# Kernel optimization log

Hardware: AMD Instinct MI355X
Metric: run time of the kernel (lower is better)

Reference implementation:

```python
import jax, jax.numpy as jnp
import numpy as np

B, T, N_EMBD, HEAD = 8, 2048, 1024, 64


def setup_inputs() -> dict:
    key = jax.random.key(0)
    kx, kq, kk, kv = jax.random.split(key, 4)
    s = 1.0 / np.sqrt(N_EMBD)
    return {
        "x": jax.random.normal(kx, (B, T, N_EMBD), dtype=jnp.float32),
        "Wq": jax.random.normal(kq, (N_EMBD, HEAD), dtype=jnp.float32) * s,
        "Wk": jax.random.normal(kk, (N_EMBD, HEAD), dtype=jnp.float32) * s,
        "Wv": jax.random.normal(kv, (N_EMBD, HEAD), dtype=jnp.float32) * s,
    }


def reference(x, Wq, Wk, Wv):
    # x: [B, T, C] with C = n_embd
    Bs, Ts, C = x.shape
    q = jnp.einsum('btc,ch->bth', x, Wq)  # [B,T,H]
    k = jnp.einsum('btc,ch->bth', x, Wk)
    v = jnp.einsum('btc,ch->bth', x, Wv)
    # NOTE: original scales by C**-0.5 where C = n_embd (input dim), not head_size
    scale = jnp.asarray(C, x.dtype) ** -0.5
    wei = jnp.einsum('bth,bsh->bts', q, k) * scale  # [B,T,T]
    causal = jnp.tril(jnp.ones((Ts, Ts), dtype=bool))
    wei = jnp.where(causal, wei, jnp.asarray(-jnp.inf, wei.dtype))
    wei = jax.nn.softmax(wei, axis=-1)
    out = jnp.einsum('bts,bsh->bth', wei, v)  # [B,T,H]
    return out
```

## Files before the change

kernel.cpp:

```cpp
#include <hip/hip_runtime.h>
#include <hip/hip_bf16.h>
#include <math.h>

#define B_ 8
#define T_ 2048
#define C_ 1024
#define H_ 64

typedef __attribute__((ext_vector_type(8))) __bf16 bf16x8;
typedef __attribute__((ext_vector_type(4))) float f32x4;

static __device__ inline unsigned short f2bf_u(float f) {
    __bf16 b = (__bf16)f;
    return __builtin_bit_cast(unsigned short, b);
}
static __device__ inline unsigned int pack2(float lo, float hi) {
    return (unsigned int)f2bf_u(lo) | ((unsigned int)f2bf_u(hi) << 16);
}
static __device__ inline bf16x8 cvt8(float4 a, float4 b) {
    bf16x8 w;
    w[0] = (__bf16)a.x; w[1] = (__bf16)a.y; w[2] = (__bf16)a.z; w[3] = (__bf16)a.w;
    w[4] = (__bf16)b.x; w[5] = (__bf16)b.y; w[6] = (__bf16)b.z; w[7] = (__bf16)b.w;
    return w;
}

__global__ void prep_w_kernel(const float* __restrict__ Wq,
                              const float* __restrict__ Wk,
                              const float* __restrict__ Wv,
                              unsigned short* __restrict__ Wp) {
    int idx = blockIdx.x * 256 + threadIdx.x;
    if (idx >= C_ * 192) return;
    int k = idx / 192;
    int n = idx % 192;
    const float* W = (n < 64) ? Wq : (n < 128) ? Wk : Wv;
    float val = W[k * 64 + (n & 63)];
    Wp[((size_t)(k >> 5) * 192 + n) * 32 + (k & 31)] = f2bf_u(val);
}

#define XSTR 264
__global__ __launch_bounds__(256, 4) void proj_kernel(
        const float* __restrict__ x, const unsigned short* __restrict__ Wp,
        unsigned short* __restrict__ q, unsigned short* __restrict__ k,
        unsigned short* __restrict__ vT) {
    __shared__ unsigned short xb[2][16][XSTR];
    const int wave = threadIdx.x >> 6;
    const int lane = threadIdx.x & 63;
    const int col  = lane & 15;
    const int quad = lane >> 4;
    const int row0 = blockIdx.x * 16;
    const int n0   = wave * 48;

    const int srow = threadIdx.x >> 4;
    const int sf   = (threadIdx.x & 15) * 16;
    const float* sb = x + (size_t)(row0 + srow) * C_ + sf;

    f32x4 acc[3];
    #pragma unroll
    for (int i = 0; i < 3; i++) acc[i] = (f32x4){0.f, 0.f, 0.f, 0.f};

    {
        float4 t0 = *(const float4*)(sb + 0),  t1 = *(const float4*)(sb + 4);
        float4 t2 = *(const float4*)(sb + 8),  t3 = *(const float4*)(sb + 12);
        *(bf16x8*)&xb[0][srow][sf]     = cvt8(t0, t1);
        *(bf16x8*)&xb[0][srow][sf + 8] = cvt8(t2, t3);
    }
    float4 l0 = *(const float4*)(sb + 256), l1 = *(const float4*)(sb + 260);
    float4 l2 = *(const float4*)(sb + 264), l3 = *(const float4*)(sb + 268);

    const unsigned short* wb = Wp + (size_t)(n0 + col) * 32 + quad * 8;
    bf16x8 bcur0 = *(const bf16x8*)(wb);
    bf16x8 bcur1 = *(const bf16x8*)(wb + 16 * 32);
    bf16x8 bcur2 = *(const bf16x8*)(wb + 32 * 32);
    __syncthreads();

    for (int p = 0; p < 4; ++p) {
        float4 f0, f1, f2, f3;
        if (p + 2 < 4) {
            const float* s2 = sb + (p + 2) * 256;
            f0 = *(const float4*)(s2 + 0);  f1 = *(const float4*)(s2 + 4);
            f2 = *(const float4*)(s2 + 8);  f3 = *(const float4*)(s2 + 12);
        }
        #pragma unroll
        for (int kt = 0; kt < 8; ++kt) {
            const int ktg = p * 8 + kt;
            bf16x8 bn0, bn1, bn2;
            if (ktg + 1 < 32) {
                const unsigned short* wn = wb + (size_t)(ktg + 1) * 192 * 32;
                bn0 = *(const bf16x8*)(wn);
                bn1 = *(const bf16x8*)(wn + 16 * 32);
                bn2 = *(const bf16x8*)(wn + 32 * 32);
            }
            bf16x8 a = *(const bf16x8*)&xb[p & 1][col][kt * 32 + quad * 8];
            acc[0] = __builtin_amdgcn_mfma_f32_16x16x32_bf16(a, bcur0, acc[0], 0, 0, 0);
            acc[1] = __builtin_amdgcn_mfma_f32_16x16x32_bf16(a, bcur1, acc[1], 0, 0, 0);
            acc[2] = __builtin_amdgcn_mfma_f32_16x16x32_bf16(a, bcur2, acc[2], 0, 0, 0);
            bcur0 = bn0; bcur1 = bn1; bcur2 = bn2;
        }
        if (p + 1 < 4) {
            unsigned short* d = &xb[(p + 1) & 1][srow][sf];
            *(bf16x8*)(d)     = cvt8(l0, l1);
            *(bf16x8*)(d + 8) = cvt8(l2, l3);
            l0 = f0; l1 = f1; l2 = f2; l3 = f3;
        }
        __syncthreads();
    }

    #pragma unroll
    for (int nt = 0; nt < 3; nt++) {
        f32x4 s = acc[nt];
        int c = n0 + nt * 16;
        int g = c >> 6;
        if (g < 2) {
            unsigned short* dst = (g == 0) ? q : k;
            int cc = (c & 63) + col;
            int grow = row0 + quad * 4;
            #pragma unroll
            for (int r = 0; r < 4; r++)
                dst[(size_t)(grow + r) * 64 + cc] = f2bf_u(s[r]);
        } else {
            int hh = (c - 128) + col;
            int bi = row0 >> 11, trow = (row0 & 2047) + quad * 4;
            ushort4 pk;
            pk.x = f2bf_u(s[0]); pk.y = f2bf_u(s[1]);
            pk.z = f2bf_u(s[2]); pk.w = f2bf_u(s[3]);
            *(ushort4*)(vT + ((size_t)bi * 64 + hh) * T_ + trow) = pk;
        }
    }
}

__global__ __launch_bounds__(512, 2) void attn_kernel(
        const unsigned short* __restrict__ q, const unsigned short* __restrict__ k,
        const unsigned short* __restrict__ vT, float* __restrict__ out) {
    __shared__ unsigned int tbuf[8][2][16 * 20];
    __shared__ float so[8][16][68];
    __shared__ float sl[8][16];
    const int wave = threadIdx.x >> 6;
    const int lane = threadIdx.x & 63;
    const int col  = lane & 15;
    const int quad = lane >> 4;
    const int bi = blockIdx.x & 7;
    const int ti = 127 - (blockIdx.x >> 3);
    const int t0 = ti * 16;
    const unsigned short* qb = q  + (size_t)bi * T_ * 64;
    const unsigned short* kb = k  + (size_t)bi * T_ * 64;
    const unsigned short* vb = vT + (size_t)bi * 64 * T_;

    bf16x8 qf0 = *(const bf16x8*)(qb + (size_t)(t0 + col) * 64 + quad * 8);
    bf16x8 qf1 = *(const bf16x8*)(qb + (size_t)(t0 + col) * 64 + 32 + quad * 8);

    f32x4 o[4];
    #pragma unroll
    for (int i = 0; i < 4; i++) o[i] = (f32x4){0.f, 0.f, 0.f, 0.f};
    float lacc = 0.f;
    const float cs = 0.03125f * 1.44269504088896f;
    const int qrow = t0 + col;

    const int nit = (t0 + 47) >> 5;
    const int ci  = (nit + 7) >> 3;
    const int it0 = wave * ci;
    const int it1 = min(it0 + ci, nit);

    for (int it = it0; it < it1; ++it) {
        const int s0 = it * 32;
        bf16x8 kf00 = *(const bf16x8*)(kb + (size_t)(s0 + col) * 64 + quad * 8);
        bf16x8 kf01 = *(const bf16x8*)(kb + (size_t)(s0 + col) * 64 + 32 + quad * 8);
        bf16x8 kf10 = *(const bf16x8*)(kb + (size_t)(s0 + 16 + col) * 64 + quad * 8);
        bf16x8 kf11 = *(const bf16x8*)(kb + (size_t)(s0 + 16 + col) * 64 + 32 + quad * 8);
        f32x4 sa = (f32x4){0.f, 0.f, 0.f, 0.f};
        f32x4 sb2 = (f32x4){0.f, 0.f, 0.f, 0.f};
        sa  = __builtin_amdgcn_mfma_f32_16x16x32_bf16(kf00, qf0, sa, 0, 0, 0);
        sa  = __builtin_amdgcn_mfma_f32_16x16x32_bf16(kf01, qf1, sa, 0, 0, 0);
        sb2 = __builtin_amdgcn_mfma_f32_16x16x32_bf16(kf10, qf0, sb2, 0, 0, 0);
        sb2 = __builtin_amdgcn_mfma_f32_16x16x32_bf16(kf11, qf1, sb2, 0, 0, 0);

        float pa[4], pb[4];
        #pragma unroll
        for (int r = 0; r < 4; r++) {
            int ka = s0 + quad * 4 + r;
            pa[r] = (ka      <= qrow) ? exp2f(sa[r]  * cs) : 0.f;
            pb[r] = (ka + 16 <= qrow) ? exp2f(sb2[r] * cs) : 0.f;
            lacc += pa[r] + pb[r];
        }
        unsigned int* tb = &tbuf[wave][it & 1][0];
        *(uint2*)&tb[col * 20 + 2 * quad] =
            make_uint2(pack2(pa[0], pa[1]), pack2(pa[2], pa[3]));
        *(uint2*)&tb[col * 20 + 8 + 2 * quad] =
            make_uint2(pack2(pb[0], pb[1]), pack2(pb[2], pb[3]));
        bf16x8 pf = *(const bf16x8*)&tb[col * 20 + 4 * quad];
        #pragma unroll
        for (int ht = 0; ht < 4; ht++) {
            bf16x8 vf = *(const bf16x8*)(vb + (size_t)(ht * 16 + col) * T_ + s0 + quad * 8);
            o[ht] = __builtin_amdgcn_mfma_f32_16x16x32_bf16(vf, pf, o[ht], 0, 0, 0);
        }
    }

    lacc += __shfl_xor(lacc, 16);
    lacc += __shfl_xor(lacc, 32);
    if (quad == 0) sl[wave][col] = lacc;
    #pragma unroll
    for (int ht = 0; ht < 4; ht++)
        *(f32x4*)&so[wave][col][ht * 16 + quad * 4] = o[ht];
    __syncthreads();

    for (int e = threadIdx.x; e < 1024; e += 512) {
        int qq = e >> 6, h = e & 63;
        float L = 0.f, val = 0.f;
        #pragma unroll
        for (int w = 0; w < 8; w++) { L += sl[w][qq]; val += so[w][qq][h]; }
        out[((size_t)bi * T_ + t0 + qq) * 64 + h] = val / L;
    }
}

extern "C" void kernel_launch(void* const* d_in, const int* in_sizes, int n_in,
                              void* d_out, int out_size, void* d_ws, size_t ws_size,
                              hipStream_t stream) {
    const float* x  = (const float*)d_in[0];
    const float* Wq = (const float*)d_in[1];
    const float* Wk = (const float*)d_in[2];
    const float* Wv = (const float*)d_in[3];
    float* out = (float*)d_out;

    unsigned short* Wp  = (unsigned short*)d_ws;
    unsigned short* qws = (unsigned short*)((char*)d_ws + 0x60000);
    unsigned short* kws = (unsigned short*)((char*)d_ws + 0x60000 + 0x200000);
    unsigned short* vws = (unsigned short*)((char*)d_ws + 0x60000 + 0x400000);

    prep_w_kernel<<<(C_ * 192 + 255) / 256, 256, 0, stream>>>(Wq, Wk, Wv, Wp);
    proj_kernel<<<(B_ * T_) / 16, 256, 0, stream>>>(x, Wp, qws, kws, vws);
    attn_kernel<<<(B_ * T_) / 16, 512, 0, stream>>>(qws, kws, vws, out);
}
```

Before: 159.2 us.

## Stage x via direct global-to-LDS loads and prefetch K/V in attention

The projection kernel now stages raw fp32 x tiles into a triple-buffered LDS ring with global_load_lds and converts to bf16 at fragment-read time. This removes the register round-trip and the separate convert-and-store step, but doubles the LDS footprint and lowers the occupancy bound to 3. The attention kernel software-pipelines K and V fragment loads one iteration ahead, skips Q loads for idle waves, and raises its occupancy hint to 4. The extra prefetch registers add register pressure.

```diff
diff --git a/kernel.cpp b/kernel.cpp
--- a/kernel.cpp
+++ b/kernel.cpp
@@ -37,12 +37,12 @@
     Wp[((size_t)(k >> 5) * 192 + n) * 32 + (k & 31)] = f2bf_u(val);
 }
 
-#define XSTR 264
-__global__ __launch_bounds__(256, 4) void proj_kernel(
+#define XROWB 1040
+__global__ __launch_bounds__(256, 3) void proj_kernel(
         const float* __restrict__ x, const unsigned short* __restrict__ Wp,
         unsigned short* __restrict__ q, unsigned short* __restrict__ k,
         unsigned short* __restrict__ vT) {
-    __shared__ unsigned short xb[2][16][XSTR];
+    __shared__ __align__(16) char xraw[3][16][XROWB];
     const int wave = threadIdx.x >> 6;
     const int lane = threadIdx.x & 63;
     const int col  = lane & 15;
@@ -50,23 +50,24 @@
     const int row0 = blockIdx.x * 16;
     const int n0   = wave * 48;
 
-    const int srow = threadIdx.x >> 4;
-    const int sf   = (threadIdx.x & 15) * 16;
-    const float* sb = x + (size_t)(row0 + srow) * C_ + sf;
+    auto stage = [&](int p, int buf) {
+        #pragma unroll
+        for (int i = 0; i < 4; i++) {
+            int r = wave * 4 + i;
+            const float* src = x + (size_t)(row0 + r) * C_ + p * 256 + lane * 4;
+            __builtin_amdgcn_global_load_lds(
+                (const __attribute__((address_space(1))) unsigned int*)src,
+                (__attribute__((address_space(3))) unsigned int*)&xraw[buf][r][0],
+                16, 0, 0);
+        }
+    };
 
     f32x4 acc[3];
     #pragma unroll
     for (int i = 0; i < 3; i++) acc[i] = (f32x4){0.f, 0.f, 0.f, 0.f};
 
-    {
-        float4 t0 = *(const float4*)(sb + 0),  t1 = *(const float4*)(sb + 4);
-        float4 t2 = *(const float4*)(sb + 8),  t3 = *(const float4*)(sb + 12);
-        *(bf16x8*)&xb[0][srow][sf]     = cvt8(t0, t1);
-        *(bf16x8*)&xb[0][srow][sf + 8] = cvt8(t2, t3);
-    }
-    float4 l0 = *(const float4*)(sb + 256), l1 = *(const float4*)(sb + 260);
-    float4 l2 = *(const float4*)(sb + 264), l3 = *(const float4*)(sb + 268);
-
+    stage(0, 0);
+    stage(1, 1);
     const unsigned short* wb = Wp + (size_t)(n0 + col) * 32 + quad * 8;
     bf16x8 bcur0 = *(const bf16x8*)(wb);
     bf16x8 bcur1 = *(const bf16x8*)(wb + 16 * 32);
@@ -74,12 +75,8 @@
     __syncthreads();
 
     for (int p = 0; p < 4; ++p) {
-        float4 f0, f1, f2, f3;
-        if (p + 2 < 4) {
-            const float* s2 = sb + (p + 2) * 256;
-            f0 = *(const float4*)(s2 + 0);  f1 = *(const float4*)(s2 + 4);
-            f2 = *(const float4*)(s2 + 8);  f3 = *(const float4*)(s2 + 12);
-        }
+        if (p + 2 < 4) stage(p + 2, (p + 2) % 3);
+        const char* abase = &xraw[p % 3][col][quad * 32];
         #pragma unroll
         for (int kt = 0; kt < 8; ++kt) {
             const int ktg = p * 8 + kt;
@@ -90,17 +87,13 @@
                 bn1 = *(const bf16x8*)(wn + 16 * 32);
                 bn2 = *(const bf16x8*)(wn + 32 * 32);
             }
-            bf16x8 a = *(const bf16x8*)&xb[p & 1][col][kt * 32 + quad * 8];
+            float4 u0 = *(const float4*)(abase + kt * 128);
+            float4 u1 = *(const float4*)(abase + kt * 128 + 16);
+            bf16x8 a = cvt8(u0, u1);
             acc[0] = __builtin_amdgcn_mfma_f32_16x16x32_bf16(a, bcur0, acc[0], 0, 0, 0);
             acc[1] = __builtin_amdgcn_mfma_f32_16x16x32_bf16(a, bcur1, acc[1], 0, 0, 0);
             acc[2] = __builtin_amdgcn_mfma_f32_16x16x32_bf16(a, bcur2, acc[2], 0, 0, 0);
             bcur0 = bn0; bcur1 = bn1; bcur2 = bn2;
-        }
-        if (p + 1 < 4) {
-            unsigned short* d = &xb[(p + 1) & 1][srow][sf];
-            *(bf16x8*)(d)     = cvt8(l0, l1);
-            *(bf16x8*)(d + 8) = cvt8(l2, l3);
-            l0 = f0; l1 = f1; l2 = f2; l3 = f3;
         }
         __syncthreads();
     }
@@ -128,7 +121,7 @@
     }
 }
 
-__global__ __launch_bounds__(512, 2) void attn_kernel(
+__global__ __launch_bounds__(512, 4) void attn_kernel(
         const unsigned short* __restrict__ q, const unsigned short* __restrict__ k,
         const unsigned short* __restrict__ vT, float* __restrict__ out) {
     __shared__ unsigned int tbuf[8][2][16 * 20];
@@ -145,9 +138,6 @@
     const unsigned short* kb = k  + (size_t)bi * T_ * 64;
     const unsigned short* vb = vT + (size_t)bi * 64 * T_;
 
-    bf16x8 qf0 = *(const bf16x8*)(qb + (size_t)(t0 + col) * 64 + quad * 8);
-    bf16x8 qf1 = *(const bf16x8*)(qb + (size_t)(t0 + col) * 64 + 32 + quad * 8);
-
     f32x4 o[4];
     #pragma unroll
     for (int i = 0; i < 4; i++) o[i] = (f32x4){0.f, 0.f, 0.f, 0.f};
@@ -160,37 +150,60 @@
     const int it0 = wave * ci;
     const int it1 = min(it0 + ci, nit);
 
-    for (int it = it0; it < it1; ++it) {
-        const int s0 = it * 32;
-        bf16x8 kf00 = *(const bf16x8*)(kb + (size_t)(s0 + col) * 64 + quad * 8);
-        bf16x8 kf01 = *(const bf16x8*)(kb + (size_t)(s0 + col) * 64 + 32 + quad * 8);
-        bf16x8 kf10 = *(const bf16x8*)(kb + (size_t)(s0 + 16 + col) * 64 + quad * 8);
-        bf16x8 kf11 = *(const bf16x8*)(kb + (size_t)(s0 + 16 + col) * 64 + 32 + quad * 8);
-        f32x4 sa = (f32x4){0.f, 0.f, 0.f, 0.f};
-        f32x4 sb2 = (f32x4){0.f, 0.f, 0.f, 0.f};
-        sa  = __builtin_amdgcn_mfma_f32_16x16x32_bf16(kf00, qf0, sa, 0, 0, 0);
-        sa  = __builtin_amdgcn_mfma_f32_16x16x32_bf16(kf01, qf1, sa, 0, 0, 0);
-        sb2 = __builtin_amdgcn_mfma_f32_16x16x32_bf16(kf10, qf0, sb2, 0, 0, 0);
-        sb2 = __builtin_amdgcn_mfma_f32_16x16x32_bf16(kf11, qf1, sb2, 0, 0, 0);
-
-        float pa[4], pb[4];
-        #pragma unroll
-        for (int r = 0; r < 4; r++) {
-            int ka = s0 + quad * 4 + r;
-            pa[r] = (ka      <= qrow) ? exp2f(sa[r]  * cs) : 0.f;
-            pb[r] = (ka + 16 <= qrow) ? exp2f(sb2[r] * cs) : 0.f;
-            lacc += pa[r] + pb[r];
-        }
-        unsigned int* tb = &tbuf[wave][it & 1][0];
-        *(uint2*)&tb[col * 20 + 2 * quad] =
-            make_uint2(pack2(pa[0], pa[1]), pack2(pa[2], pa[3]));
-        *(uint2*)&tb[col * 20 + 8 + 2 * quad] =
-            make_uint2(pack2(pb[0], pb[1]), pack2(pb[2], pb[3]));
-        bf16x8 pf = *(const bf16x8*)&tb[col * 20 + 4 * quad];
-        #pragma unroll
-        for (int ht = 0; ht < 4; ht++) {
-            bf16x8 vf = *(const bf16x8*)(vb + (size_t)(ht * 16 + col) * T_ + s0 + quad * 8);
-            o[ht] = __builtin_amdgcn_mfma_f32_16x16x32_bf16(vf, pf, o[ht], 0, 0, 0);
+    if (it0 < it1) {
+        bf16x8 qf0 = *(const bf16x8*)(qb + (size_t)(t0 + col) * 64 + quad * 8);
+        bf16x8 qf1 = *(const bf16x8*)(qb + (size_t)(t0 + col) * 64 + 32 + quad * 8);
+
+        int s0 = it0 * 32;
+        bf16x8 kc0 = *(const bf16x8*)(kb + (size_t)(s0 + col) * 64 + quad * 8);
+        bf16x8 kc1 = *(const bf16x8*)(kb + (size_t)(s0 + col) * 64 + 32 + quad * 8);
+        bf16x8 kc2 = *(const bf16x8*)(kb + (size_t)(s0 + 16 + col) * 64 + quad * 8);
+        bf16x8 kc3 = *(const bf16x8*)(kb + (size_t)(s0 + 16 + col) * 64 + 32 + quad * 8);
+        bf16x8 vc[4];
+        #pragma unroll
+        for (int ht = 0; ht < 4; ht++)
+            vc[ht] = *(const bf16x8*)(vb + (size_t)(ht * 16 + col) * T_ + s0 + quad * 8);
+
+        for (int it = it0; it < it1; ++it) {
+            s0 = it * 32;
+            const int sn = min(it + 1, it1 - 1) * 32;
+            bf16x8 kn0 = *(const bf16x8*)(kb + (size_t)(sn + col) * 64 + quad * 8);
+            bf16x8 kn1 = *(const bf16x8*)(kb + (size_t)(sn + col) * 64 + 32 + quad * 8);
+            bf16x8 kn2 = *(const bf16x8*)(kb + (size_t)(sn + 16 + col) * 64 + quad * 8);
+            bf16x8 kn3 = *(const bf16x8*)(kb + (size_t)(sn + 16 + col) * 64 + 32 + quad * 8);
+            bf16x8 vn[4];
+            #pragma unroll
+            for (int ht = 0; ht < 4; ht++)
+                vn[ht] = *(const bf16x8*)(vb + (size_t)(ht * 16 + col) * T_ + sn + quad * 8);
+
+            f32x4 sa = (f32x4){0.f, 0.f, 0.f, 0.f};
+            f32x4 sb = (f32x4){0.f, 0.f, 0.f, 0.f};
+            sa = __builtin_amdgcn_mfma_f32_16x16x32_bf16(kc0, qf0, sa, 0, 0, 0);
+            sa = __builtin_amdgcn_mfma_f32_16x16x32_bf16(kc1, qf1, sa, 0, 0, 0);
+            sb = __builtin_amdgcn_mfma_f32_16x16x32_bf16(kc2, qf0, sb, 0, 0, 0);
+            sb = __builtin_amdgcn_mfma_f32_16x16x32_bf16(kc3, qf1, sb, 0, 0, 0);
+
+            float pa[4], pb[4];
+            #pragma unroll
+            for (int r = 0; r < 4; r++) {
+                int ka = s0 + quad * 4 + r;
+                pa[r] = (ka      <= qrow) ? exp2f(sa[r] * cs) : 0.f;
+                pb[r] = (ka + 16 <= qrow) ? exp2f(sb[r] * cs) : 0.f;
+                lacc += pa[r] + pb[r];
+            }
+            unsigned int* tb = &tbuf[wave][it & 1][0];
+            *(uint2*)&tb[col * 20 + 2 * quad] =
+                make_uint2(pack2(pa[0], pa[1]), pack2(pa[2], pa[3]));
+            *(uint2*)&tb[col * 20 + 8 + 2 * quad] =
+                make_uint2(pack2(pb[0], pb[1]), pack2(pb[2], pb[3]));
+            bf16x8 pf = *(const bf16x8*)&tb[col * 20 + 4 * quad];
+            #pragma unroll
+            for (int ht = 0; ht < 4; ht++)
+                o[ht] = __builtin_amdgcn_mfma_f32_16x16x32_bf16(vc[ht], pf, o[ht], 0, 0, 0);
+
+            kc0 = kn0; kc1 = kn1; kc2 = kn2; kc3 = kn3;
+            #pragma unroll
+            for (int ht = 0; ht < 4; ht++) vc[ht] = vn[ht];
         }
     }
 
```

Measured after the change: 165.5 us. 1.04x slower.
